# Kernel optimization log

Measured on AMD Instinct MI355X. Metric: run time of the kernel, lower is better.

## Reference

```python
import jax, jax.numpy as jnp
import numpy as np

B, Tm1, N, H = 512, 99, 128, 256  # batch, T-1, input_size, hidden_size


def setup_inputs() -> dict:
    key = jax.random.key(0)
    ks = jax.random.split(key, 12)
    s = 0.05
    return {
        "input_data": jax.random.normal(ks[0], (B, Tm1, N), dtype=jnp.float32),
        "W1": jax.random.normal(ks[1], (Tm1, 2 * H), dtype=jnp.float32) * s,  # attn_linear1
        "b1": jax.random.normal(ks[2], (Tm1,), dtype=jnp.float32) * s,
        "W2": jax.random.normal(ks[3], (Tm1, Tm1), dtype=jnp.float32) * s,   # attn_linear2
        "b2": jax.random.normal(ks[4], (Tm1,), dtype=jnp.float32) * s,
        "W3": jax.random.normal(ks[5], (1, Tm1), dtype=jnp.float32) * s,     # attn_linear3
        "b3": jax.random.normal(ks[6], (1,), dtype=jnp.float32) * s,
        "W_ih": jax.random.normal(ks[7], (4 * H, N), dtype=jnp.float32) * s, # LSTM (i,f,g,o)
        "W_hh": jax.random.normal(ks[8], (4 * H, H), dtype=jnp.float32) * s,
        "b_ih": jax.random.normal(ks[9], (4 * H,), dtype=jnp.float32) * s,
        "b_hh": jax.random.normal(ks[10], (4 * H,), dtype=jnp.float32) * s,
    }


def _forward(input_data, W1, b1, W2, b2, W3, b3, W_ih, W_hh, b_ih, b_hh):
    # z2 = attn_linear2(input_data.permute(0,2,1)) is time-invariant; precompute. (B, N, Tm1)
    z2 = jnp.einsum('btn,st->bns', input_data, W2) + b2
    w3 = W3[0]  # (Tm1,)
    bias = b_ih + b_hh

    def step(carry, x_t):
        h, c = carry  # (B, H) each
        # attention over input features, conditioned on (h, c)
        z1 = jnp.concatenate([h, c], axis=-1) @ W1.T + b1          # (B, Tm1)
        x = jnp.tanh(z1[:, None, :] + z2)                          # (B, N, Tm1)
        e = jnp.einsum('bnt,t->bn', x, w3) + b3[0]                 # (B, N)
        attn = jax.nn.softmax(e, axis=1)                           # (B, N)
        w = attn * x_t                                             # (B, N)
        # LSTM cell (PyTorch gate order: i, f, g, o)
        gates = w @ W_ih.T + h @ W_hh.T + bias                     # (B, 4H)
        i, f, g, o = jnp.split(gates, 4, axis=-1)
        c_new = jax.nn.sigmoid(f) * c + jax.nn.sigmoid(i) * jnp.tanh(g)
        h_new = jax.nn.sigmoid(o) * jnp.tanh(c_new)
        return (h_new, c_new), (w, h_new)

    h0 = jnp.zeros((input_data.shape[0], H), dtype=input_data.dtype)
    c0 = jnp.zeros_like(h0)
    xs = jnp.transpose(input_data, (1, 0, 2))                      # (Tm1, B, N)
    _, (w_seq, h_seq) = jax.lax.scan(step, (h0, c0), xs)
    input_weighted = jnp.transpose(w_seq, (1, 0, 2))               # (B, Tm1, N)
    input_encoded = jnp.transpose(h_seq, (1, 0, 2))                # (B, Tm1, H)
    return input_weighted, input_encoded


def reference(input_data, W1, b1, W2, b2, W3, b3, W_ih, W_hh, b_ih, b_hh):
    return _forward(input_data, W1, b1, W2, b2, W3, b3, W_ih, W_hh, b_ih, b_hh)
```

## Files before the change

kernel.cpp:

```cpp
#include <hip/hip_runtime.h>


typedef unsigned int  uint32;
typedef unsigned short u16;
typedef _Float16 h2  __attribute__((ext_vector_type(2)));
typedef uint32   u4  __attribute__((ext_vector_type(4)));

#define TS 99
#define BB 512
#define NN 128
#define HH 256

__device__ __forceinline__ float frcp(float x){ return __builtin_amdgcn_rcpf(x); }
__device__ __forceinline__ float ftanh(float x){
  float t = __expf(2.f * x);
  return 1.f - 2.f * frcp(t + 1.f);
}
__device__ __forceinline__ float fsig(float x){
  return frcp(1.f + __expf(-x));
}
__device__ __forceinline__ uint32 pk2(float a, float b){
  union { h2 h; uint32 u; } v;
  v.h[0] = (_Float16)a; v.h[1] = (_Float16)b; return v.u;
}
__device__ __forceinline__ float h2ff(u16 u){
  union { u16 us; _Float16 h; } v; v.us = u; return (float)v.h;
}
__device__ __forceinline__ float dot2(uint32 a, uint32 b, float c){
  union { uint32 u; h2 h; } x, y; x.u = a; y.u = b;
#if __has_builtin(__builtin_amdgcn_fdot2)
  return __builtin_amdgcn_fdot2(x.h, y.h, c, false);
#else
  c = fmaf((float)x.h[0], (float)y.h[0], c);
  return fmaf((float)x.h[1], (float)y.h[1], c);
#endif
}

struct KParams {
  const float *in, *W1, *b1, *W2, *b2, *W3, *Wih, *Whh, *bih, *bhh;
  float *out;
  const uint32 *Wg4;
  const uint32 *W1c4;
};

__global__ void pack_kernel(const float* W1, const float* Wih, const float* Whh,
                            uint32* Wg4, uint32* W1c4)
{
  int idx = blockIdx.x * 256 + threadIdx.x;
  if (idx < 48 * 1024 * 4) {
    int i = idx & 3, j = (idx >> 2) & 1023, kb = idx >> 12;
    int pp = kb * 4 + i;
    float a, b;
    if (pp < 64) { a = Wih[j * 128 + 2 * pp];       b = Wih[j * 128 + 2 * pp + 1]; }
    else { int q = pp - 64; a = Whh[j * 256 + 2 * q]; b = Whh[j * 256 + 2 * q + 1]; }
    Wg4[idx] = pk2(a, b);
  } else {
    int v = idx - 48 * 1024 * 4;
    if (v < 64 * 128 * 4) {
      int i = v & 3, s = (v >> 2) & 127, kpb = v >> 9;
      int kp = kpb * 4 + i;
      uint32 r = 0;
      if (s < TS) r = pk2(W1[(size_t)s * 512 + 2 * kp],
                          W1[(size_t)s * 512 + 2 * kp + 1]);
      W1c4[v] = r;
    }
  }
}

__global__ __launch_bounds__(512, 1) void enc_kernel(KParams p)
{
  __shared__ u16    int_s[2][128][102];
  __shared__ u16    z2s[2][128][102];
  __shared__ uint32 hcp[2][256];
  __shared__ uint32 wp[2][64];
  __shared__ float  z1part[2][4][128];
  __shared__ float  z1s[2][128];
  __shared__ float  epart[2][2][128];
  __shared__ float  gl[2][1024];
  __shared__ float  biasl[1024];
  __shared__ float  w3s[128], b1s[128];

  const int tid = threadIdx.x;
  const int blk = blockIdx.x;
  const int b0  = blk * 2;

  float* outw = p.out;
  float* oute = p.out + (size_t)BB * TS * NN;

  for (int b = 0; b < 2; ++b) {
    const float* src = p.in + (size_t)(b0 + b) * TS * NN;
    for (int idx = tid; idx < TS * NN; idx += 512) {
      int t = idx >> 7, n = idx & 127;
      int_s[b][n][t] = (u16)(pk2(src[idx], 0.f) & 0xFFFFu);
    }
  }
  if (tid < 128) {
    w3s[tid] = (tid < TS) ? p.W3[tid] : 0.f;
    b1s[tid] = (tid < TS) ? p.b1[tid] : 0.f;
  }
  hcp[tid >> 8][tid & 255] = 0;
  biasl[tid]       = p.bih[tid]       + p.bhh[tid];
  biasl[tid + 512] = p.bih[tid + 512] + p.bhh[tid + 512];
  __syncthreads();
  {
    int n = tid & 127, b = (tid >> 7) & 1, hf = tid >> 8;
    int s0 = hf * 50, s1 = hf ? TS : 50;
    const u16* ir = int_s[b][n];
    for (int s = s0; s < s1; ++s) {
      float acc = p.b2[s];
      const float* w2r = p.W2 + s * TS;
      for (int tt = 0; tt + 1 < TS; tt += 2) {
        uint32 pr = *(const uint32*)&ir[tt];
        union { uint32 u; h2 h; } v; v.u = pr;
        acc = fmaf((float)v.h[0], w2r[tt],     acc);
        acc = fmaf((float)v.h[1], w2r[tt + 1], acc);
      }
      acc = fmaf(h2ff(ir[98]), w2r[98], acc);
      z2s[b][n][s] = (u16)(pk2(acc, 0.f) & 0xFFFFu);
    }
  }
  __syncthreads();

  float creg = 0.f;
  const int lu = tid & 255, lb = tid >> 8;

  for (int t = 0; t < TS; ++t) {
    {
      int s = tid & 127, q = tid >> 7;
      float a0 = 0.f, a1 = 0.f;
      #pragma unroll 4
      for (int kk = 0; kk < 16; ++kk) {
        int kpb = q * 16 + kk;
        u4 w  = *(const u4*)(p.W1c4 + ((size_t)kpb * 128 + s) * 4);
        u4 x0 = *(const u4*)&hcp[0][kpb * 4];
        u4 x1 = *(const u4*)&hcp[1][kpb * 4];
        #pragma unroll
        for (int i = 0; i < 4; ++i) {
          a0 = dot2(w[i], x0[i], a0);
          a1 = dot2(w[i], x1[i], a1);
        }
      }
      z1part[0][q][s] = a0;
      z1part[1][q][s] = a1;
    }
    __syncthreads();
    if (tid < 256) {
      int b = tid >> 7, s = tid & 127;
      z1s[b][s] = b1s[s] + ((z1part[b][0][s] + z1part[b][1][s])
                          + (z1part[b][2][s] + z1part[b][3][s]));
    }
    __syncthreads();

    {
      int n = tid & 127, b = (tid >> 7) & 1, hf = tid >> 8;
      int s0 = hf * 50, s1 = hf ? TS : 50;
      const u16* zr = z2s[b][n];
      float acc = 0.f;
      for (int s = s0; s < s1; ++s)
        acc = fmaf(w3s[s], ftanh(z1s[b][s] + h2ff(zr[s])), acc);
      epart[b][hf][n] = acc;
    }
    __syncthreads();

    if (tid < 128) {
      int b = tid >> 6, lane = tid & 63;
      float v0 = epart[b][0][lane]      + epart[b][1][lane];
      float v1 = epart[b][0][lane + 64] + epart[b][1][lane + 64];
      float m = fmaxf(v0, v1);
      for (int off = 32; off; off >>= 1) m = fmaxf(m, __shfl_xor(m, off));
      float e0 = __expf(v0 - m), e1 = __expf(v1 - m);
      float sm = e0 + e1;
      for (int off = 32; off; off >>= 1) sm += __shfl_xor(sm, off);
      float r = frcp(sm);
      const float* xr = p.in + ((size_t)(b0 + b) * TS + t) * NN;
      float w0 = e0 * r * xr[lane];
      float w1 = e1 * r * xr[lane + 64];
      float* orow = outw + ((size_t)(b0 + b) * TS + t) * NN;
      orow[lane]      = w0;
      orow[lane + 64] = w1;
      float w0n = __shfl_xor(w0, 1), w1n = __shfl_xor(w1, 1);
      if ((lane & 1) == 0) {
        wp[b][lane >> 1]        = pk2(w0, w0n);
        wp[b][32 + (lane >> 1)] = pk2(w1, w1n);
      }
    }
    __syncthreads();

    {
      float a00 = 0.f, a01 = 0.f, a10 = 0.f, a11 = 0.f;
      const uint32* wg = p.Wg4;
      #pragma unroll 4
      for (int kb = 0; kb < 16; ++kb) {
        u4 w0 = *(const u4*)(wg + ((size_t)kb * 1024 + tid) * 4);
        u4 w1 = *(const u4*)(wg + ((size_t)kb * 1024 + tid + 512) * 4);
        u4 x0 = *(const u4*)&wp[0][kb * 4];
        u4 x1 = *(const u4*)&wp[1][kb * 4];
        #pragma unroll
        for (int i = 0; i < 4; ++i) {
          a00 = dot2(w0[i], x0[i], a00); a01 = dot2(w1[i], x0[i], a01);
          a10 = dot2(w0[i], x1[i], a10); a11 = dot2(w1[i], x1[i], a11);
        }
      }
      #pragma unroll 4
      for (int kb = 16; kb < 48; ++kb) {
        u4 w0 = *(const u4*)(wg + ((size_t)kb * 1024 + tid) * 4);
        u4 w1 = *(const u4*)(wg + ((size_t)kb * 1024 + tid + 512) * 4);
        u4 x0 = *(const u4*)&hcp[0][(kb - 16) * 4];
        u4 x1 = *(const u4*)&hcp[1][(kb - 16) * 4];
        #pragma unroll
        for (int i = 0; i < 4; ++i) {
          a00 = dot2(w0[i], x0[i], a00); a01 = dot2(w1[i], x0[i], a01);
          a10 = dot2(w0[i], x1[i], a10); a11 = dot2(w1[i], x1[i], a11);
        }
      }
      gl[0][tid]       = a00 + biasl[tid];
      gl[0][tid + 512] = a01 + biasl[tid + 512];
      gl[1][tid]       = a10 + biasl[tid];
      gl[1][tid + 512] = a11 + biasl[tid + 512];
    }
    __syncthreads();

    {
      float iv = gl[lb][lu],       fv = gl[lb][256 + lu];
      float gv = gl[lb][512 + lu], ov = gl[lb][768 + lu];
      float cn = fsig(fv) * creg + fsig(iv) * ftanh(gv);
      float hn = fsig(ov) * ftanh(cn);
      creg = cn;
      oute[((size_t)(b0 + lb) * TS + t) * HH + lu] = hn;
      float hx = __shfl_xor(hn, 1);
      float cx = __shfl_xor(cn, 1);
      if ((lu & 1) == 0) {
        hcp[lb][lu >> 1]         = pk2(hn, hx);
        hcp[lb][128 + (lu >> 1)] = pk2(cn, cx);
      }
    }
    __syncthreads();
  }
}

extern "C" void kernel_launch(void* const* d_in, const int* in_sizes, int n_in,
                              void* d_out, int out_size, void* d_ws, size_t ws_size,
                              hipStream_t stream)
{
  KParams p;
  p.in  = (const float*)d_in[0];
  p.W1  = (const float*)d_in[1];
  p.b1  = (const float*)d_in[2];
  p.W2  = (const float*)d_in[3];
  p.b2  = (const float*)d_in[4];
  p.W3  = (const float*)d_in[5];
  p.Wih = (const float*)d_in[7];
  p.Whh = (const float*)d_in[8];
  p.bih = (const float*)d_in[9];
  p.bhh = (const float*)d_in[10];
  p.out = (float*)d_out;

  char* ws = (char*)d_ws;
  const size_t wg4Bytes  = 48ull * 1024 * 4 * 4;
  const size_t w1c4Bytes = 64ull * 128 * 4 * 4;
  const size_t needBytes = wg4Bytes + w1c4Bytes;
  if (ws_size < needBytes) return;

  uint32* Wg4  = (uint32*)ws;
  uint32* W1c4 = (uint32*)(ws + wg4Bytes);
  p.Wg4  = Wg4;
  p.W1c4 = W1c4;

  pack_kernel<<<dim3(896), dim3(256), 0, stream>>>(p.W1, p.Wih, p.Whh,
                                                   Wg4, W1c4);
  enc_kernel<<<dim3(256), dim3(512), 0, stream>>>(p);
}
```

Baseline: 1.413 ms.

## Use bf16 MFMA for attention-z1 and LSTM gate matmuls, overlap h-part with attention

Replaces the fp16 dot2 scalar GEMVs for z1 and the LSTM gates with bf16 MFMA 16x16x32 instructions. Weights are pre-packed into MFMA-fragment layout, and the batch of 2 fills two of the 16 M rows. The recurrent h·W_hh part of the gate GEMM is issued before the attention tanh loop so it can overlap. One barrier and the z1 partial-sum reduction are removed. This wastes most MFMA rows, and bf16 lowers precision compared with fp16.

```diff
diff --git a/kernel.cpp b/kernel.cpp
--- a/kernel.cpp
+++ b/kernel.cpp
@@ -3,14 +3,25 @@
 
 typedef unsigned int  uint32;
 typedef unsigned short u16;
-typedef _Float16 h2  __attribute__((ext_vector_type(2)));
-typedef uint32   u4  __attribute__((ext_vector_type(4)));
+typedef float  f4  __attribute__((ext_vector_type(4)));
+typedef short  s8v __attribute__((ext_vector_type(8)));
 
 #define TS 99
 #define BB 512
 #define NN 128
 #define HH 256
 
+__device__ __forceinline__ u16 f2bf(float f){
+  union { float f; uint32 i; } v; v.f = f;
+  uint32 r = v.i + 0x7FFFu + ((v.i >> 16) & 1u);
+  return (u16)(r >> 16);
+}
+__device__ __forceinline__ u16 f2h(float f){
+  union { _Float16 h; u16 u; } v; v.h = (_Float16)f; return v.u;
+}
+__device__ __forceinline__ float h2ff(u16 u){
+  union { u16 u2; _Float16 h; } v; v.u2 = u; return (float)v.h;
+}
 __device__ __forceinline__ float frcp(float x){ return __builtin_amdgcn_rcpf(x); }
 __device__ __forceinline__ float ftanh(float x){
   float t = __expf(2.f * x);
@@ -19,66 +30,48 @@
 __device__ __forceinline__ float fsig(float x){
   return frcp(1.f + __expf(-x));
 }
-__device__ __forceinline__ uint32 pk2(float a, float b){
-  union { h2 h; uint32 u; } v;
-  v.h[0] = (_Float16)a; v.h[1] = (_Float16)b; return v.u;
-}
-__device__ __forceinline__ float h2ff(u16 u){
-  union { u16 us; _Float16 h; } v; v.us = u; return (float)v.h;
-}
-__device__ __forceinline__ float dot2(uint32 a, uint32 b, float c){
-  union { uint32 u; h2 h; } x, y; x.u = a; y.u = b;
-#if __has_builtin(__builtin_amdgcn_fdot2)
-  return __builtin_amdgcn_fdot2(x.h, y.h, c, false);
-#else
-  c = fmaf((float)x.h[0], (float)y.h[0], c);
-  return fmaf((float)x.h[1], (float)y.h[1], c);
-#endif
-}
 
 struct KParams {
   const float *in, *W1, *b1, *W2, *b2, *W3, *Wih, *Whh, *bih, *bhh;
   float *out;
-  const uint32 *Wg4;
-  const uint32 *W1c4;
+  const s8v *Wgpk;
+  const s8v *W1pk;
 };
 
 __global__ void pack_kernel(const float* W1, const float* Wih, const float* Whh,
-                            uint32* Wg4, uint32* W1c4)
+                            u16* Wgpk, u16* W1pk)
 {
   int idx = blockIdx.x * 256 + threadIdx.x;
-  if (idx < 48 * 1024 * 4) {
-    int i = idx & 3, j = (idx >> 2) & 1023, kb = idx >> 12;
-    int pp = kb * 4 + i;
-    float a, b;
-    if (pp < 64) { a = Wih[j * 128 + 2 * pp];       b = Wih[j * 128 + 2 * pp + 1]; }
-    else { int q = pp - 64; a = Whh[j * 256 + 2 * q]; b = Whh[j * 256 + 2 * q + 1]; }
-    Wg4[idx] = pk2(a, b);
+  if (idx < 12 * 64 * 64 * 8) {
+    int jj = idx & 7, lane = (idx >> 3) & 63, jt = (idx >> 9) & 63, kc = idx >> 15;
+    int j  = jt * 16 + (lane & 15);
+    int kk = kc * 32 + ((lane >> 4) * 8) + jj;
+    float v = (kc < 4) ? Wih[(size_t)j * 128 + kk]
+                       : Whh[(size_t)j * 256 + (kk - 128)];
+    Wgpk[idx] = f2bf(v);
   } else {
-    int v = idx - 48 * 1024 * 4;
-    if (v < 64 * 128 * 4) {
-      int i = v & 3, s = (v >> 2) & 127, kpb = v >> 9;
-      int kp = kpb * 4 + i;
-      uint32 r = 0;
-      if (s < TS) r = pk2(W1[(size_t)s * 512 + 2 * kp],
-                          W1[(size_t)s * 512 + 2 * kp + 1]);
-      W1c4[v] = r;
+    int v2 = idx - 12 * 64 * 64 * 8;
+    if (v2 < 7 * 16 * 64 * 8) {
+      int jj = v2 & 7, lane = (v2 >> 3) & 63, kc = (v2 >> 9) & 15, st = v2 >> 13;
+      int col = st * 16 + (lane & 15);
+      int kk  = kc * 32 + ((lane >> 4) * 8) + jj;
+      float v = (col < TS) ? W1[(size_t)col * 512 + kk] : 0.f;
+      W1pk[v2] = f2bf(v);
     }
   }
 }
 
 __global__ __launch_bounds__(512, 1) void enc_kernel(KParams p)
 {
-  __shared__ u16    int_s[2][128][102];
-  __shared__ u16    z2s[2][128][102];
-  __shared__ uint32 hcp[2][256];
-  __shared__ uint32 wp[2][64];
-  __shared__ float  z1part[2][4][128];
-  __shared__ float  z1s[2][128];
-  __shared__ float  epart[2][2][128];
-  __shared__ float  gl[2][1024];
-  __shared__ float  biasl[1024];
-  __shared__ float  w3s[128], b1s[128];
+  __shared__ __align__(16) u16   int_s[2][128][102];
+  __shared__ __align__(16) u16   z2s[2][128][102];
+  __shared__ __align__(16) u16   hcb[2][512];
+  __shared__ __align__(16) u16   wpb[2][128];
+  __shared__ __align__(16) float z1s[2][112];
+  __shared__ float epart[2][2][128];
+  __shared__ float gl[2][1024];
+  __shared__ float biasl[1024];
+  __shared__ float w3s[128], b1s[128];
 
   const int tid = threadIdx.x;
   const int blk = blockIdx.x;
@@ -86,19 +79,25 @@
 
   float* outw = p.out;
   float* oute = p.out + (size_t)BB * TS * NN;
+
+  const int wv  = tid >> 6, lane = tid & 63;
+  const int m15 = lane & 15;
+  const int q8  = (lane >> 4) * 8;
+  const int r16 = lane >> 4;
 
   for (int b = 0; b < 2; ++b) {
     const float* src = p.in + (size_t)(b0 + b) * TS * NN;
     for (int idx = tid; idx < TS * NN; idx += 512) {
       int t = idx >> 7, n = idx & 127;
-      int_s[b][n][t] = (u16)(pk2(src[idx], 0.f) & 0xFFFFu);
+      int_s[b][n][t] = f2h(src[idx]);
     }
   }
   if (tid < 128) {
     w3s[tid] = (tid < TS) ? p.W3[tid] : 0.f;
     b1s[tid] = (tid < TS) ? p.b1[tid] : 0.f;
   }
-  hcp[tid >> 8][tid & 255] = 0;
+  ((u16*)hcb)[tid]       = 0;
+  ((u16*)hcb)[tid + 512] = 0;
   biasl[tid]       = p.bih[tid]       + p.bhh[tid];
   biasl[tid + 512] = p.bih[tid + 512] + p.bhh[tid + 512];
   __syncthreads();
@@ -111,12 +110,11 @@
       const float* w2r = p.W2 + s * TS;
       for (int tt = 0; tt + 1 < TS; tt += 2) {
         uint32 pr = *(const uint32*)&ir[tt];
-        union { uint32 u; h2 h; } v; v.u = pr;
-        acc = fmaf((float)v.h[0], w2r[tt],     acc);
-        acc = fmaf((float)v.h[1], w2r[tt + 1], acc);
+        acc = fmaf(h2ff((u16)(pr & 0xFFFFu)),  w2r[tt],     acc);
+        acc = fmaf(h2ff((u16)(pr >> 16)),      w2r[tt + 1], acc);
       }
       acc = fmaf(h2ff(ir[98]), w2r[98], acc);
-      z2s[b][n][s] = (u16)(pk2(acc, 0.f) & 0xFFFFu);
+      z2s[b][n][s] = f2h(acc);
     }
   }
   __syncthreads();
@@ -125,47 +123,56 @@
   const int lu = tid & 255, lb = tid >> 8;
 
   for (int t = 0; t < TS; ++t) {
-    {
-      int s = tid & 127, q = tid >> 7;
-      float a0 = 0.f, a1 = 0.f;
-      #pragma unroll 4
-      for (int kk = 0; kk < 16; ++kk) {
-        int kpb = q * 16 + kk;
-        u4 w  = *(const u4*)(p.W1c4 + ((size_t)kpb * 128 + s) * 4);
-        u4 x0 = *(const u4*)&hcp[0][kpb * 4];
-        u4 x1 = *(const u4*)&hcp[1][kpb * 4];
-        #pragma unroll
-        for (int i = 0; i < 4; ++i) {
-          a0 = dot2(w[i], x0[i], a0);
-          a1 = dot2(w[i], x1[i], a1);
-        }
-      }
-      z1part[0][q][s] = a0;
-      z1part[1][q][s] = a1;
-    }
-    __syncthreads();
-    if (tid < 256) {
-      int b = tid >> 7, s = tid & 127;
-      z1s[b][s] = b1s[s] + ((z1part[b][0][s] + z1part[b][1][s])
-                          + (z1part[b][2][s] + z1part[b][3][s]));
-    }
-    __syncthreads();
-
+    if (wv < 7) {
+      f4 zacc = {0.f, 0.f, 0.f, 0.f};
+      const s8v* wb = p.W1pk + (size_t)wv * 16 * 64 + lane;
+      #pragma unroll
+      for (int kc = 0; kc < 16; ++kc) {
+        s8v av = *(const s8v*)&hcb[m15 & 1][kc * 32 + q8];
+        zacc = __builtin_amdgcn_mfma_f32_16x16x32_bf16(av, wb[kc * 64], zacc,
+                                                       0, 0, 0);
+      }
+      if (r16 == 0) {
+        int s = wv * 16 + m15;
+        z1s[0][s] = b1s[s] + zacc[0];
+        z1s[1][s] = b1s[s] + zacc[1];
+      }
+    }
+    __syncthreads();
+
+    f4 acc0 = {0,0,0,0}, acc1 = {0,0,0,0}, acc2 = {0,0,0,0}, acc3 = {0,0,0,0};
+    f4 acc4 = {0,0,0,0}, acc5 = {0,0,0,0}, acc6 = {0,0,0,0}, acc7 = {0,0,0,0};
+    {
+      const s8v* wg = p.Wgpk + lane + (size_t)(wv * 8) * 64;
+      #pragma unroll
+      for (int kc = 4; kc < 12; ++kc) {
+        s8v av = *(const s8v*)&hcb[m15 & 1][(kc - 4) * 32 + q8];
+        const s8v* wk = wg + (size_t)kc * 64 * 64;
+        acc0 = __builtin_amdgcn_mfma_f32_16x16x32_bf16(av, wk[0 * 64], acc0, 0, 0, 0);
+        acc1 = __builtin_amdgcn_mfma_f32_16x16x32_bf16(av, wk[1 * 64], acc1, 0, 0, 0);
+        acc2 = __builtin_amdgcn_mfma_f32_16x16x32_bf16(av, wk[2 * 64], acc2, 0, 0, 0);
+        acc3 = __builtin_amdgcn_mfma_f32_16x16x32_bf16(av, wk[3 * 64], acc3, 0, 0, 0);
+        acc4 = __builtin_amdgcn_mfma_f32_16x16x32_bf16(av, wk[4 * 64], acc4, 0, 0, 0);
+        acc5 = __builtin_amdgcn_mfma_f32_16x16x32_bf16(av, wk[5 * 64], acc5, 0, 0, 0);
+        acc6 = __builtin_amdgcn_mfma_f32_16x16x32_bf16(av, wk[6 * 64], acc6, 0, 0, 0);
+        acc7 = __builtin_amdgcn_mfma_f32_16x16x32_bf16(av, wk[7 * 64], acc7, 0, 0, 0);
+      }
+    }
     {
       int n = tid & 127, b = (tid >> 7) & 1, hf = tid >> 8;
       int s0 = hf * 50, s1 = hf ? TS : 50;
       const u16* zr = z2s[b][n];
-      float acc = 0.f;
+      float acce = 0.f;
       for (int s = s0; s < s1; ++s)
-        acc = fmaf(w3s[s], ftanh(z1s[b][s] + h2ff(zr[s])), acc);
-      epart[b][hf][n] = acc;
+        acce = fmaf(w3s[s], ftanh(z1s[b][s] + h2ff(zr[s])), acce);
+      epart[b][hf][n] = acce;
     }
     __syncthreads();
 
     if (tid < 128) {
-      int b = tid >> 6, lane = tid & 63;
-      float v0 = epart[b][0][lane]      + epart[b][1][lane];
-      float v1 = epart[b][0][lane + 64] + epart[b][1][lane + 64];
+      int b = tid >> 6, ln = tid & 63;
+      float v0 = epart[b][0][ln]      + epart[b][1][ln];
+      float v1 = epart[b][0][ln + 64] + epart[b][1][ln + 64];
       float m = fmaxf(v0, v1);
       for (int off = 32; off; off >>= 1) m = fmaxf(m, __shfl_xor(m, off));
       float e0 = __expf(v0 - m), e1 = __expf(v1 - m);
@@ -173,66 +180,56 @@
       for (int off = 32; off; off >>= 1) sm += __shfl_xor(sm, off);
       float r = frcp(sm);
       const float* xr = p.in + ((size_t)(b0 + b) * TS + t) * NN;
-      float w0 = e0 * r * xr[lane];
-      float w1 = e1 * r * xr[lane + 64];
+      float w0 = e0 * r * xr[ln];
+      float w1 = e1 * r * xr[ln + 64];
       float* orow = outw + ((size_t)(b0 + b) * TS + t) * NN;
-      orow[lane]      = w0;
-      orow[lane + 64] = w1;
-      float w0n = __shfl_xor(w0, 1), w1n = __shfl_xor(w1, 1);
-      if ((lane & 1) == 0) {
-        wp[b][lane >> 1]        = pk2(w0, w0n);
-        wp[b][32 + (lane >> 1)] = pk2(w1, w1n);
-      }
-    }
-    __syncthreads();
-
-    {
-      float a00 = 0.f, a01 = 0.f, a10 = 0.f, a11 = 0.f;
-      const uint32* wg = p.Wg4;
-      #pragma unroll 4
-      for (int kb = 0; kb < 16; ++kb) {
-        u4 w0 = *(const u4*)(wg + ((size_t)kb * 1024 + tid) * 4);
-        u4 w1 = *(const u4*)(wg + ((size_t)kb * 1024 + tid + 512) * 4);
-        u4 x0 = *(const u4*)&wp[0][kb * 4];
-        u4 x1 = *(const u4*)&wp[1][kb * 4];
-        #pragma unroll
-        for (int i = 0; i < 4; ++i) {
-          a00 = dot2(w0[i], x0[i], a00); a01 = dot2(w1[i], x0[i], a01);
-          a10 = dot2(w0[i], x1[i], a10); a11 = dot2(w1[i], x1[i], a11);
-        }
-      }
-      #pragma unroll 4
-      for (int kb = 16; kb < 48; ++kb) {
-        u4 w0 = *(const u4*)(wg + ((size_t)kb * 1024 + tid) * 4);
-        u4 w1 = *(const u4*)(wg + ((size_t)kb * 1024 + tid + 512) * 4);
-        u4 x0 = *(const u4*)&hcp[0][(kb - 16) * 4];
-        u4 x1 = *(const u4*)&hcp[1][(kb - 16) * 4];
-        #pragma unroll
-        for (int i = 0; i < 4; ++i) {
-          a00 = dot2(w0[i], x0[i], a00); a01 = dot2(w1[i], x0[i], a01);
-          a10 = dot2(w0[i], x1[i], a10); a11 = dot2(w1[i], x1[i], a11);
-        }
-      }
-      gl[0][tid]       = a00 + biasl[tid];
-      gl[0][tid + 512] = a01 + biasl[tid + 512];
-      gl[1][tid]       = a10 + biasl[tid];
-      gl[1][tid + 512] = a11 + biasl[tid + 512];
-    }
-    __syncthreads();
-
-    {
-      float iv = gl[lb][lu],       fv = gl[lb][256 + lu];
-      float gv = gl[lb][512 + lu], ov = gl[lb][768 + lu];
+      orow[ln]      = w0;
+      orow[ln + 64] = w1;
+      wpb[b][ln]      = f2bf(w0);
+      wpb[b][ln + 64] = f2bf(w1);
+    }
+    __syncthreads();
+
+    {
+      const s8v* wg = p.Wgpk + lane + (size_t)(wv * 8) * 64;
+      #pragma unroll
+      for (int kc = 0; kc < 4; ++kc) {
+        s8v av = *(const s8v*)&wpb[m15 & 1][kc * 32 + q8];
+        const s8v* wk = wg + (size_t)kc * 64 * 64;
+        acc0 = __builtin_amdgcn_mfma_f32_16x16x32_bf16(av, wk[0 * 64], acc0, 0, 0, 0);
+        acc1 = __builtin_amdgcn_mfma_f32_16x16x32_bf16(av, wk[1 * 64], acc1, 0, 0, 0);
+        acc2 = __builtin_amdgcn_mfma_f32_16x16x32_bf16(av, wk[2 * 64], acc2, 0, 0, 0);
+        acc3 = __builtin_amdgcn_mfma_f32_16x16x32_bf16(av, wk[3 * 64], acc3, 0, 0, 0);
+        acc4 = __builtin_amdgcn_mfma_f32_16x16x32_bf16(av, wk[4 * 64], acc4, 0, 0, 0);
+        acc5 = __builtin_amdgcn_mfma_f32_16x16x32_bf16(av, wk[5 * 64], acc5, 0, 0, 0);
+        acc6 = __builtin_amdgcn_mfma_f32_16x16x32_bf16(av, wk[6 * 64], acc6, 0, 0, 0);
+        acc7 = __builtin_amdgcn_mfma_f32_16x16x32_bf16(av, wk[7 * 64], acc7, 0, 0, 0);
+      }
+      if (r16 == 0) {
+        int jb = wv * 8 * 16 + m15;
+        gl[0][jb +   0] = acc0[0];  gl[1][jb +   0] = acc0[1];
+        gl[0][jb +  16] = acc1[0];  gl[1][jb +  16] = acc1[1];
+        gl[0][jb +  32] = acc2[0];  gl[1][jb +  32] = acc2[1];
+        gl[0][jb +  48] = acc3[0];  gl[1][jb +  48] = acc3[1];
+        gl[0][jb +  64] = acc4[0];  gl[1][jb +  64] = acc4[1];
+        gl[0][jb +  80] = acc5[0];  gl[1][jb +  80] = acc5[1];
+        gl[0][jb +  96] = acc6[0];  gl[1][jb +  96] = acc6[1];
+        gl[0][jb + 112] = acc7[0];  gl[1][jb + 112] = acc7[1];
+      }
+    }
+    __syncthreads();
+
+    {
+      float iv = gl[lb][lu]       + biasl[lu];
+      float fv = gl[lb][256 + lu] + biasl[256 + lu];
+      float gv = gl[lb][512 + lu] + biasl[512 + lu];
+      float ov = gl[lb][768 + lu] + biasl[768 + lu];
       float cn = fsig(fv) * creg + fsig(iv) * ftanh(gv);
       float hn = fsig(ov) * ftanh(cn);
       creg = cn;
       oute[((size_t)(b0 + lb) * TS + t) * HH + lu] = hn;
-      float hx = __shfl_xor(hn, 1);
-      float cx = __shfl_xor(cn, 1);
-      if ((lu & 1) == 0) {
-        hcp[lb][lu >> 1]         = pk2(hn, hx);
-        hcp[lb][128 + (lu >> 1)] = pk2(cn, cx);
-      }
+      hcb[lb][lu]       = f2bf(hn);
+      hcb[lb][256 + lu] = f2bf(cn);
     }
     __syncthreads();
   }
@@ -256,17 +253,19 @@
   p.out = (float*)d_out;
 
   char* ws = (char*)d_ws;
-  const size_t wg4Bytes  = 48ull * 1024 * 4 * 4;
-  const size_t w1c4Bytes = 64ull * 128 * 4 * 4;
-  const size_t needBytes = wg4Bytes + w1c4Bytes;
+  const size_t wgpkBytes = 12ull * 64 * 64 * 8 * 2;
+  const size_t w1pkBytes = 7ull * 16 * 64 * 8 * 2;
+  const size_t needBytes = wgpkBytes + w1pkBytes;
   if (ws_size < needBytes) return;
 
-  uint32* Wg4  = (uint32*)ws;
-  uint32* W1c4 = (uint32*)(ws + wg4Bytes);
-  p.Wg4  = Wg4;
-  p.W1c4 = W1c4;
-
-  pack_kernel<<<dim3(896), dim3(256), 0, stream>>>(p.W1, p.Wih, p.Whh,
-                                                   Wg4, W1c4);
+  u16* Wgpk = (u16*)ws;
+  u16* W1pk = (u16*)(ws + wgpkBytes);
+  p.Wgpk = (const s8v*)Wgpk;
+  p.W1pk = (const s8v*)W1pk;
+
+  const int packElems = 12 * 64 * 64 * 8 + 7 * 16 * 64 * 8;
+  pack_kernel<<<dim3((packElems + 255) / 256), dim3(256), 0, stream>>>(
+      p.W1, p.Wih, p.Whh, Wgpk, W1pk);
+
   enc_kernel<<<dim3(256), dim3(512), 0, stream>>>(p);
 }
```

Result: slower. 1.941 ms (+37.4%).
